# Kernel optimization log

Hardware: AMD Instinct MI355X
Metric: run time of the kernel (lower is better)

## Reference

```python
import jax, jax.numpy as jnp
import numpy as np

N_RAYS, MAX_S, N_VOX, EMB, HID, L_VIEW = 8192, 64, 100000, 32, 128, 4


def view_pe(d):
    # NeRF positional encoding of view dirs: [N,3] -> [N, 3 + 6*L_VIEW]
    freqs = 2.0 ** jnp.arange(L_VIEW, dtype=d.dtype)
    ang = (d[..., None] * freqs).reshape(*d.shape[:-1], -1)  # [N, 3*L]
    return jnp.concatenate([d, jnp.sin(ang), jnp.cos(ang)], -1)


def setup_inputs() -> dict:
    key = jax.random.key(0)
    ks = jax.random.split(key, 16)
    rays_d = jax.random.normal(ks[0], (N_RAYS, 3), dtype=jnp.float32)
    rays_d = rays_d / jnp.linalg.norm(rays_d, axis=-1, keepdims=True)
    pts = jax.random.uniform(ks[1], (N_RAYS, MAX_S, 3), dtype=jnp.float32)
    t_vals = jnp.sort(jax.random.uniform(ks[2], (N_RAYS, MAX_S), dtype=jnp.float32) * 4.0, axis=-1)
    dists = jnp.concatenate([t_vals[:, 1:] - t_vals[:, :-1], jnp.full((N_RAYS, 1), 0.05, jnp.float32)], -1)
    # ragged per-ray sample counts -> -1 padded p2v_idx (as produced by the voxel point sampler)
    counts = jax.random.randint(ks[3], (N_RAYS,), 1, MAX_S + 1)
    ray_hits = jax.random.bernoulli(ks[4], 0.9, (N_RAYS,))
    valid = (jnp.arange(MAX_S)[None, :] < counts[:, None]) & ray_hits[:, None]
    idx = jax.random.randint(ks[5], (N_RAYS, MAX_S), 0, N_VOX)
    p2v_idx = jnp.where(valid, idx, -1).astype(jnp.int32)

    def lin(k, i, o):
        return jax.random.normal(k, (i, o), dtype=jnp.float32) * np.float32(1.0 / np.sqrt(i))

    return dict(
        rays_d=rays_d, pts=pts, t_vals=t_vals, dists=dists,
        p2v_idx=p2v_idx, ray_hits=ray_hits,
        vox_emb=jax.random.normal(ks[6], (N_VOX, EMB), dtype=jnp.float32) * 0.1,
        Wpts=lin(ks[7], 3, EMB),
        W1=lin(ks[8], EMB, HID), b1=jnp.zeros((HID,), jnp.float32),
        W2=lin(ks[9], HID, HID), b2=jnp.zeros((HID,), jnp.float32),
        Wsig=lin(ks[10], HID, 1), bsig=jnp.zeros((1,), jnp.float32),
        Wfeat=lin(ks[11], HID, HID), bfeat=jnp.zeros((HID,), jnp.float32),
        Wc1=lin(ks[12], HID + 3 + 6 * L_VIEW, 64), bc1=jnp.zeros((64,), jnp.float32),
        Wc2=lin(ks[13], 64, 3), bc2=jnp.zeros((3,), jnp.float32),
    )


def reference(rays_d, pts, t_vals, dists, vox_emb, Wpts, W1, b1, W2, b2,
              Wsig, bsig, Wfeat, bfeat, Wc1, bc1, Wc2, bc2, p2v_idx, ray_hits):
    mask = p2v_idx >= 0                                   # [N,S] valid samples (mask_pts)
    idx = jnp.where(mask, p2v_idx, 0)
    # voxel_embedder: per-point voxel embedding gather + positional lift
    ve = vox_emb[idx] + pts @ Wpts                        # [N,S,EMB]
    h = jax.nn.relu(ve @ W1 + b1)
    h = jax.nn.relu(h @ W2 + b2)                          # [N,S,HID]
    sigma = (h @ Wsig + bsig)[..., 0]                     # [N,S]
    feat = h @ Wfeat + bfeat                              # [N,S,HID]
    vemb = view_pe(rays_d)                                # [N,27]
    vemb = jnp.broadcast_to(vemb[:, None, :], (feat.shape[0], feat.shape[1], vemb.shape[-1]))
    c = jax.nn.relu(jnp.concatenate([feat, vemb], -1) @ Wc1 + bc1)
    rgb_raw = c @ Wc2 + bc2                               # [N,S,3]
    # masked_scatter semantics: invalid slots are 0 before the min_color remap
    rgb = (jnp.where(mask[..., None], rgb_raw, 0.0) + 1.0) * 0.5   # min_color = -1
    free_energy = jnp.where(mask, jax.nn.relu(sigma) * dists, 0.0)  # [N,S]
    # volumetric_rendering(with_dist=True)
    shifted = jnp.concatenate([jnp.zeros_like(free_energy[:, :1]), free_energy[:, :-1]], -1)
    T = jnp.exp(-jnp.cumsum(shifted, -1))
    weights = (1.0 - jnp.exp(-free_energy)) * T           # [N,S]
    comp_rgb = jnp.einsum('ns,nsc->nc', weights, rgb)     # [N,3]
    acc = weights.sum(-1)                                 # [N]
    depth = (weights * t_vals).sum(-1)
    disp = 1.0 / jnp.maximum(1e-10, depth / jnp.maximum(acc, 1e-10))
    # fill_in for missed rays (white_bkgd=False -> fill with 0)
    comp_rgb = jnp.where(ray_hits[:, None], comp_rgb, 0.0)
    disp = jnp.where(ray_hits, disp, 0.0)
    acc = jnp.where(ray_hits, acc, 0.0)
    return comp_rgb, disp, acc
```

## Files before the change

### kernel.cpp

```cpp
#include <hip/hip_runtime.h>
#include <stdint.h>


#define NRAYS 8192
#define MAXS  64
#define EMB   32
#define HID   128
#define NPE   27
#define CH    64
#define NPTS  (NRAYS * MAXS)
#define RCAP  16384

#define WS_WCOMB  0
#define WS_WPE    (WS_WCOMB + HID*CH)
#define WS_BCOMB  (WS_WPE + 32*CH)
#define WS_CCINIT (WS_BCOMB + CH)
#define WS_COUNTS (WS_CCINIT + NRAYS*CH)
#define WS_OFFS   (WS_COUNTS + NRAYS)
#define WS_TOTAL  (WS_OFFS + NRAYS)
#define WS_RCNT   (WS_TOTAL + 1)
#define WS_LIST   (WS_TOTAL + 4)
#define WS_PTOUT  (WS_LIST + NPTS)
#define WS_FRAGS  (WS_PTOUT + 4*NPTS)
#define WS_RLIST  (WS_FRAGS + 56*2*64*4)
#define WS_PTSC   (WS_RLIST + RCAP)

typedef __attribute__((ext_vector_type(8))) short bf16x8;
typedef __attribute__((ext_vector_type(4))) float f32x4;
union FI { int i[4]; int4 v; bf16x8 f; };

#define MFMA16(a, b, c) __builtin_amdgcn_mfma_f32_16x16x32_bf16(a, b, c, 0, 0, 0)

__device__ __forceinline__ f32x4 mfma3(bf16x8 ah, bf16x8 al, bf16x8 bh, bf16x8 bl,
                                       f32x4 c) {
  c = MFMA16(al, bh, c);
  c = MFMA16(ah, bl, c);
  c = MFMA16(ah, bh, c);
  return c;
}

__device__ __forceinline__ f32x4 mfma2(bf16x8 ah, bf16x8 bh, bf16x8 bl, f32x4 c) {
  c = MFMA16(ah, bl, c);
  c = MFMA16(ah, bh, c);
  return c;
}

__device__ __forceinline__ void split8(const float* x, bf16x8& hi, bf16x8& lo) {
  FI H, L;
#pragma unroll
  for (int r = 0; r < 4; ++r) {
    unsigned u0 = __float_as_uint(x[2 * r]);
    unsigned u1 = __float_as_uint(x[2 * r + 1]);
    unsigned h0 = u0 & 0xffff0000u, h1 = u1 & 0xffff0000u;
    unsigned l0 = __float_as_uint(x[2 * r] - __uint_as_float(h0));
    unsigned l1 = __float_as_uint(x[2 * r + 1] - __uint_as_float(h1));
    H.i[r] = (int)((h0 >> 16) | (h1 & 0xffff0000u));
    L.i[r] = (int)((l0 >> 16) | (l1 & 0xffff0000u));
  }
  hi = H.f; lo = L.f;
}

__device__ __forceinline__ unsigned short bf16rne(float v) {
  unsigned u = __float_as_uint(v);
  return (unsigned short)((u + 0x7fffu + ((u >> 16) & 1u)) >> 16);
}

__global__ __launch_bounds__(256) void prep_kernel(
    const float* __restrict__ Wfeat, const float* __restrict__ bfeat,
    const float* __restrict__ Wc1, const float* __restrict__ bc1,
    float* __restrict__ ws) {
  int idx = blockIdx.x * 256 + threadIdx.x;
  if (idx < HID * CH) {
    int m = idx >> 6, j = idx & 63;
    float s = 0.f;
    for (int f = 0; f < HID; ++f) s = fmaf(Wfeat[m * HID + f], Wc1[f * CH + j], s);
    ws[WS_WCOMB + idx] = s;
    return;
  }
  idx -= HID * CH;
  if (idx < 32 * CH) {
    int v = idx >> 6, j = idx & 63;
    ws[WS_WPE + idx] = (v < NPE) ? Wc1[(HID + v) * CH + j] : 0.f;
    return;
  }
  idx -= 32 * CH;
  if (idx < CH) {
    float s = bc1[idx];
    for (int f = 0; f < HID; ++f) s = fmaf(bfeat[f], Wc1[f * CH + idx], s);
    ws[WS_BCOMB + idx] = s;
    return;
  }
  idx -= CH;
  if (idx < 2) ((int*)(ws + WS_TOTAL))[idx] = 0;
}

__global__ __launch_bounds__(256) void prep2_kernel(
    const float* __restrict__ W1, const float* __restrict__ W2,
    float* __restrict__ ws) {
  int t = blockIdx.x * 256 + threadIdx.x;
  if (t >= 56 * 64) return;
  const int fid = t >> 6, lane = t & 63;
  const int n16 = lane & 15, quad = lane >> 4;
  float x[8];
  if (fid < 8) {
    const int n = fid * 16 + n16, k0 = quad * 8;
#pragma unroll
    for (int j = 0; j < 8; ++j) x[j] = W1[(k0 + j) * HID + n];
  } else if (fid < 40) {
    const int f = fid - 8, nt = f >> 2, s = f & 3;
    const int n = nt * 16 + n16, k0 = s * 32 + quad * 8;
#pragma unroll
    for (int j = 0; j < 8; ++j) x[j] = W2[(k0 + j) * HID + n];
  } else {
    const int f = fid - 40, nt = f >> 2, s = f & 3;
    const int n = nt * 16 + n16, k0 = s * 32 + quad * 8;
#pragma unroll
    for (int j = 0; j < 8; ++j) x[j] = ws[WS_WCOMB + (k0 + j) * CH + n];
  }
  FI H, L;
#pragma unroll
  for (int r = 0; r < 4; ++r) {
    unsigned u0 = __float_as_uint(x[2 * r]);
    unsigned u1 = __float_as_uint(x[2 * r + 1]);
    unsigned h0 = u0 & 0xffff0000u, h1 = u1 & 0xffff0000u;
    unsigned l0 = __float_as_uint(x[2 * r] - __uint_as_float(h0));
    unsigned l1 = __float_as_uint(x[2 * r + 1] - __uint_as_float(h1));
    H.i[r] = (int)((h0 >> 16) | (h1 & 0xffff0000u));
    L.i[r] = (int)((l0 >> 16) | (l1 & 0xffff0000u));
  }
  int4* o = (int4*)(ws + WS_FRAGS);
  o[(fid * 2 + 0) * 64 + lane] = H.v;
  o[(fid * 2 + 1) * 64 + lane] = L.v;
}

__global__ __launch_bounds__(256) void count_pe_kernel(
    const float* __restrict__ rays_d, const int* __restrict__ p2v,
    float* __restrict__ ws) {
  const int tid = threadIdx.x;
  const int ray = blockIdx.x * 4 + (tid >> 6);
  const int lane = tid & 63;
  const int v = p2v[ray * MAXS + lane];
  const unsigned long long ball = __ballot(v >= 0);
  if (lane == 0) ((int*)(ws + WS_COUNTS))[ray] = __popcll(ball);

  const float d0 = rays_d[ray * 3 + 0];
  const float d1 = rays_d[ray * 3 + 1];
  const float d2 = rays_d[ray * 3 + 2];
  float vemb[NPE];
  vemb[0] = d0; vemb[1] = d1; vemb[2] = d2;
#pragma unroll
  for (int i = 0; i < 3; ++i) {
    const float di = (i == 0) ? d0 : (i == 1) ? d1 : d2;
#pragma unroll
    for (int l = 0; l < 4; ++l) {
      const float ang = di * (float)(1 << l);
      vemb[3 + i * 4 + l] = __sinf(ang);
      vemb[3 + 12 + i * 4 + l] = __cosf(ang);
    }
  }
  float s = ws[WS_BCOMB + lane];
  const float* wpe = ws + WS_WPE;
#pragma unroll
  for (int vv = 0; vv < NPE; ++vv) s = fmaf(vemb[vv], wpe[vv * CH + lane], s);
  ws[WS_CCINIT + ray * CH + lane] = s;
}

__global__ __launch_bounds__(1024) void scan_kernel(float* __restrict__ ws) {
  const int* counts = (const int*)(ws + WS_COUNTS);
  int* offs = (int*)(ws + WS_OFFS);
  int* totalp = (int*)(ws + WS_TOTAL);
  __shared__ int wsum[16];
  const int tid = threadIdx.x;
  const int lane = tid & 63;
  const int base = tid * 8;
  if (tid == 0) ((int*)(ws + WS_RCNT))[0] = 0;
  int c[8], e[8];
  int run = 0;
#pragma unroll
  for (int i = 0; i < 8; ++i) { c[i] = counts[base + i]; e[i] = run; run += c[i]; }
  int inc = run;
#pragma unroll
  for (int off = 1; off < 64; off <<= 1) {
    int u = __shfl_up(inc, off, 64);
    if (lane >= off) inc += u;
  }
  const int wexcl = inc - run;
  if (lane == 63) wsum[tid >> 6] = inc;
  __syncthreads();
  if (tid < 16) {
    int v = wsum[tid];
    int inc2 = v;
#pragma unroll
    for (int off = 1; off < 16; off <<= 1) {
      int u = __shfl_up(inc2, off, 64);
      if (tid >= off) inc2 += u;
    }
    wsum[tid] = inc2 - v;
    if (tid == 15) totalp[0] = inc2;
  }
  __syncthreads();
  const int wbase = wsum[tid >> 6];
#pragma unroll
  for (int i = 0; i < 8; ++i) offs[base + i] = wbase + wexcl + e[i];
}

__global__ __launch_bounds__(256) void list_kernel(
    const int* __restrict__ p2v, const float* __restrict__ pts,
    float* __restrict__ ws) {
  const int tid = threadIdx.x;
  const int ray = blockIdx.x * 4 + (tid >> 6);
  const int lane = tid & 63;
  const int pidx = ray * MAXS + lane;
  const int gidx = p2v[pidx];
  const bool valid = gidx >= 0;
  const unsigned long long ball = __ballot(valid);
  const int rank = __popcll(ball & ((1ull << lane) - 1ull));
  if (valid) {
    const int off = ((const int*)(ws + WS_OFFS))[ray];
    const int slot = off + rank;
    ((int*)(ws + WS_LIST))[slot] = pidx;
    float4 pc;
    pc.x = pts[pidx * 3 + 0];
    pc.y = pts[pidx * 3 + 1];
    pc.z = pts[pidx * 3 + 2];
    pc.w = __int_as_float(gidx);
    ((float4*)(ws + WS_PTSC))[slot] = pc;
  }
}

__device__ __forceinline__ void ve_frag(const float* __restrict__ vox_emb,
                                        const float* __restrict__ Wpts,
                                        float4 pc, int quad,
                                        bf16x8& hi, bf16x8& lo) {
  float x[8];
  const int gidx = __float_as_int(pc.w);
  const float4* vr = (const float4*)vox_emb + gidx * 8 + quad * 2;
  const float4 va = vr[0], vb = vr[1];
  const float px = pc.x, py = pc.y, pz = pc.z;
  const float4* wp = (const float4*)Wpts;
  const float4 wa0 = wp[quad * 2 + 0], wa1 = wp[quad * 2 + 1];
  const float4 wb0 = wp[8 + quad * 2 + 0], wb1 = wp[8 + quad * 2 + 1];
  const float4 wc0 = wp[16 + quad * 2 + 0], wc1 = wp[16 + quad * 2 + 1];
  x[0] = va.x + fmaf(px, wa0.x, fmaf(py, wb0.x, pz * wc0.x));
  x[1] = va.y + fmaf(px, wa0.y, fmaf(py, wb0.y, pz * wc0.y));
  x[2] = va.z + fmaf(px, wa0.z, fmaf(py, wb0.z, pz * wc0.z));
  x[3] = va.w + fmaf(px, wa0.w, fmaf(py, wb0.w, pz * wc0.w));
  x[4] = vb.x + fmaf(px, wa1.x, fmaf(py, wb1.x, pz * wc1.x));
  x[5] = vb.y + fmaf(px, wa1.y, fmaf(py, wb1.y, pz * wc1.y));
  x[6] = vb.z + fmaf(px, wa1.z, fmaf(py, wb1.z, pz * wc1.z));
  x[7] = vb.w + fmaf(px, wa1.w, fmaf(py, wb1.w, pz * wc1.w));
  split8(x, hi, lo);
}

#define SROW 136

__global__ __launch_bounds__(128, 2) void mlp_mfma(
    const float* __restrict__ vox_emb, const float* __restrict__ Wpts,
    const float* __restrict__ b1, const float* __restrict__ b2,
    const float* __restrict__ Wsig, const float* __restrict__ bsig,
    const float* __restrict__ Wc2, const float* __restrict__ bc2,
    float* __restrict__ ws) {
  __shared__ __align__(16) unsigned short alds[64 * SROW];
  const int tid = threadIdx.x;
  const int wave = tid >> 6, lane = tid & 63;
  const int n16 = lane & 15, quad = lane >> 4;
  const int total = ((const int*)(ws + WS_TOTAL))[0];
  const int base = blockIdx.x * 64 + wave * 32;
  if (base >= total) return;
  const int* list = (const int*)(ws + WS_LIST);
  const int slot0 = min(base + n16, total - 1);
  const int slot1 = min(base + 16 + n16, total - 1);
  const int pidx0 = list[slot0];
  const int pidx1 = list[slot1];
  const float4 pc0 = ((const float4*)(ws + WS_PTSC))[slot0];
  const float4 pc1 = ((const float4*)(ws + WS_PTSC))[slot1];
  const int4* fb = (const int4*)(ws + WS_FRAGS);

  int4 B1f[16];
#pragma unroll
  for (int i = 0; i < 16; ++i) B1f[i] = fb[i * 64 + lane];

  bf16x8 a0h, a0l, a1h, a1l;
  ve_frag(vox_emb, Wpts, pc0, quad, a0h, a0l);
  ve_frag(vox_emb, Wpts, pc1, quad, a1h, a1l);

  int4 BL[2][16];
#pragma unroll
  for (int nt = 0; nt < 8; ++nt) {
    BL[0][2 * nt]     = fb[((8 + nt * 4) * 2 + 0) * 64 + lane];
    BL[0][2 * nt + 1] = fb[((8 + nt * 4) * 2 + 1) * 64 + lane];
  }

  f32x4 h[2][8];
#pragma unroll
  for (int nt = 0; nt < 8; ++nt) {
    const float bb = b1[nt * 16 + n16];
    h[0][nt] = (f32x4){bb, bb, bb, bb};
    h[1][nt] = h[0][nt];
  }
#pragma unroll
  for (int nt = 0; nt < 8; ++nt) {
    FI H, L; H.v = B1f[2 * nt]; L.v = B1f[2 * nt + 1];
    h[0][nt] = mfma3(a0h, a0l, H.f, L.f, h[0][nt]);
    h[1][nt] = mfma3(a1h, a1l, H.f, L.f, h[1][nt]);
  }
#pragma unroll
  for (int mt = 0; mt < 2; ++mt)
#pragma unroll
    for (int nt = 0; nt < 8; ++nt)
#pragma unroll
      for (int r = 0; r < 4; ++r) {
        const float v = fmaxf(h[mt][nt][r], 0.f);
        const int row = wave * 32 + mt * 16 + quad * 4 + r;
        const int gk = ((2 * nt + (n16 >> 3)) ^ (row & 7)) << 3;
        alds[row * SROW + gk + (n16 & 7)] = bf16rne(v);
      }

  f32x4 g[2][8];
#pragma unroll
  for (int nt = 0; nt < 8; ++nt) {
    const float bb = b2[nt * 16 + n16];
    g[0][nt] = (f32x4){bb, bb, bb, bb};
    g[1][nt] = g[0][nt];
  }
  const int rrow0 = (wave * 32 + n16) * SROW;
  const int rrow1 = rrow0 + 16 * SROW;
  const int t7 = n16 & 7;
#pragma unroll
  for (int s = 0; s < 4; ++s) {
    if (s < 3) {
#pragma unroll
      for (int nt = 0; nt < 8; ++nt) {
        BL[(s + 1) & 1][2 * nt]     = fb[((8 + nt * 4 + s + 1) * 2 + 0) * 64 + lane];
        BL[(s + 1) & 1][2 * nt + 1] = fb[((8 + nt * 4 + s + 1) * 2 + 1) * 64 + lane];
      }
    }
    const int gq = ((4 * s + quad) ^ t7) << 3;
    const bf16x8 A0h = *(const bf16x8*)&alds[rrow0 + gq];
    const bf16x8 A1h = *(const bf16x8*)&alds[rrow1 + gq];
#pragma unroll
    for (int nt = 0; nt < 8; ++nt) {
      FI H, L; H.v = BL[s & 1][2 * nt]; L.v = BL[s & 1][2 * nt + 1];
      g[0][nt] = mfma2(A0h, H.f, L.f, g[0][nt]);
      g[1][nt] = mfma2(A1h, H.f, L.f, g[1][nt]);
    }
  }

  int pm[2][4];
#pragma unroll
  for (int mt = 0; mt < 2; ++mt)
#pragma unroll
    for (int r = 0; r < 4; ++r)
      pm[mt][r] = __shfl(mt ? pidx1 : pidx0, quad * 4 + r, 64);
  int4 BC[2][8];
#pragma unroll
  for (int nt = 0; nt < 4; ++nt) {
    BC[0][2 * nt]     = fb[((40 + nt * 4) * 2 + 0) * 64 + lane];
    BC[0][2 * nt + 1] = fb[((40 + nt * 4) * 2 + 1) * 64 + lane];
  }
  f32x4 cacc[2][4];
#pragma unroll
  for (int mt = 0; mt < 2; ++mt)
#pragma unroll
    for (int nt = 0; nt < 4; ++nt)
#pragma unroll
      for (int r = 0; r < 4; ++r)
        cacc[mt][nt][r] = ws[WS_CCINIT + (pm[mt][r] >> 6) * CH + nt * 16 + n16];

  float sg[2][4] = {{0.f, 0.f, 0.f, 0.f}, {0.f, 0.f, 0.f, 0.f}};
#pragma unroll
  for (int nt = 0; nt < 8; ++nt) {
    const float sv = Wsig[nt * 16 + n16];
#pragma unroll
    for (int mt = 0; mt < 2; ++mt)
#pragma unroll
      for (int r = 0; r < 4; ++r) {
        const float v = fmaxf(g[mt][nt][r], 0.f);
        sg[mt][r] = fmaf(v, sv, sg[mt][r]);
        const int row = wave * 32 + mt * 16 + quad * 4 + r;
        const int gk = ((2 * nt + (n16 >> 3)) ^ (row & 7)) << 3;
        alds[row * SROW + gk + (n16 & 7)] = bf16rne(v);
      }
  }
#pragma unroll
  for (int mask = 1; mask < 16; mask <<= 1)
#pragma unroll
    for (int mt = 0; mt < 2; ++mt)
#pragma unroll
      for (int r = 0; r < 4; ++r) sg[mt][r] += __shfl_xor(sg[mt][r], mask, 64);

#pragma unroll
  for (int s = 0; s < 4; ++s) {
    if (s < 3) {
#pragma unroll
      for (int nt = 0; nt < 4; ++nt) {
        BC[(s + 1) & 1][2 * nt]     = fb[((40 + nt * 4 + s + 1) * 2 + 0) * 64 + lane];
        BC[(s + 1) & 1][2 * nt + 1] = fb[((40 + nt * 4 + s + 1) * 2 + 1) * 64 + lane];
      }
    }
    const int gq = ((4 * s + quad) ^ t7) << 3;
    const bf16x8 A0h = *(const bf16x8*)&alds[rrow0 + gq];
    const bf16x8 A1h = *(const bf16x8*)&alds[rrow1 + gq];
#pragma unroll
    for (int nt = 0; nt < 4; ++nt) {
      FI H, L; H.v = BC[s & 1][2 * nt]; L.v = BC[s & 1][2 * nt + 1];
      cacc[0][nt] = mfma2(A0h, H.f, L.f, cacc[0][nt]);
      cacc[1][nt] = mfma2(A1h, H.f, L.f, cacc[1][nt]);
    }
  }

  float cr[2][3][4];
#pragma unroll
  for (int mt = 0; mt < 2; ++mt)
#pragma unroll
    for (int c = 0; c < 3; ++c)
#pragma unroll
      for (int r = 0; r < 4; ++r) cr[mt][c][r] = 0.f;
#pragma unroll
  for (int nt = 0; nt < 4; ++nt) {
    const int j = nt * 16 + n16;
    const float w0 = Wc2[j * 3 + 0], w1c = Wc2[j * 3 + 1], w2c = Wc2[j * 3 + 2];
#pragma unroll
    for (int mt = 0; mt < 2; ++mt)
#pragma unroll
      for (int r = 0; r < 4; ++r) {
        const float cv = fmaxf(cacc[mt][nt][r], 0.f);
        cr[mt][0][r] = fmaf(cv, w0, cr[mt][0][r]);
        cr[mt][1][r] = fmaf(cv, w1c, cr[mt][1][r]);
        cr[mt][2][r] = fmaf(cv, w2c, cr[mt][2][r]);
      }
  }
#pragma unroll
  for (int mask = 1; mask < 16; mask <<= 1)
#pragma unroll
    for (int mt = 0; mt < 2; ++mt)
#pragma unroll
      for (int c = 0; c < 3; ++c)
#pragma unroll
        for (int r = 0; r < 4; ++r) cr[mt][c][r] += __shfl_xor(cr[mt][c][r], mask, 64);

  if (n16 == 0) {
    const float bs = bsig[0];
    const float bcr = bc2[0], bcg = bc2[1], bcb = bc2[2];
#pragma unroll
    for (int mt = 0; mt < 2; ++mt)
#pragma unroll
      for (int r = 0; r < 4; ++r) {
        const int m = mt * 16 + quad * 4 + r;
        if (base + m < total) {
          const int pid = pm[mt][r];
          const float sig = sg[mt][r] + bs;
          ((float4*)(ws + WS_PTOUT))[pid] =
              make_float4(sig, cr[mt][0][r] + bcr, cr[mt][1][r] + bcg, cr[mt][2][r] + bcb);
          if (fabsf(sig) < 0.006f) {
            const int ri = atomicAdd((int*)(ws + WS_RCNT), 1);
            if (ri < RCAP) ((int*)(ws + WS_RLIST))[ri] = pid;
          }
        }
      }
  }
}

__device__ __forceinline__ float wave_sum(float v) {
#pragma unroll
  for (int off = 32; off > 0; off >>= 1) v += __shfl_down(v, off, 64);
  return v;
}

__global__ __launch_bounds__(256) void repair_kernel(
    const float* __restrict__ pts, const int* __restrict__ p2v,
    const float* __restrict__ vox_emb, const float* __restrict__ Wpts,
    const float* __restrict__ W1, const float* __restrict__ b1,
    const float* __restrict__ W2, const float* __restrict__ b2,
    const float* __restrict__ Wsig, const float* __restrict__ bsig,
    float* __restrict__ ws) {
  __shared__ float h1s[4][HID];
  const int wv = threadIdx.x >> 6, lane = threadIdx.x & 63;
  const int cnt = min(((const int*)(ws + WS_RCNT))[0], RCAP);
  const int nw = gridDim.x * 4;
  for (int i = blockIdx.x * 4 + wv; i < cnt; i += nw) {
    const int pidx = ((const int*)(ws + WS_RLIST))[i];
    const int gidx = p2v[pidx];
    const float px = pts[pidx * 3 + 0];
    const float py = pts[pidx * 3 + 1];
    const float pz = pts[pidx * 3 + 2];
    float ve[EMB];
#pragma unroll
    for (int e = 0; e < EMB; ++e)
      ve[e] = vox_emb[gidx * EMB + e] +
              fmaf(px, Wpts[e], fmaf(py, Wpts[EMB + e], pz * Wpts[2 * EMB + e]));
    float s0 = b1[lane], s1 = b1[lane + 64];
#pragma unroll
    for (int k = 0; k < EMB; ++k) {
      const float x = ve[k];
      s0 = fmaf(x, W1[k * HID + lane], s0);
      s1 = fmaf(x, W1[k * HID + lane + 64], s1);
    }
    h1s[wv][lane] = fmaxf(s0, 0.f);
    h1s[wv][lane + 64] = fmaxf(s1, 0.f);
    float t0 = b2[lane], t1 = b2[lane + 64];
    for (int k = 0; k < HID; ++k) {
      const float x = h1s[wv][k];
      t0 = fmaf(x, W2[k * HID + lane], t0);
      t1 = fmaf(x, W2[k * HID + lane + 64], t1);
    }
    float sp = fmaf(fmaxf(t0, 0.f), Wsig[lane], fmaxf(t1, 0.f) * Wsig[lane + 64]);
    sp = wave_sum(sp);
    if (lane == 0) ws[WS_PTOUT + 4 * pidx + 0] = sp + bsig[0];
  }
}

__device__ __forceinline__ float wave_prefix_excl(float v, int lane) {
  float inc = v;
#pragma unroll
  for (int off = 1; off < 64; off <<= 1) {
    float u = __shfl_up(inc, off, 64);
    if (lane >= off) inc += u;
  }
  return inc - v;
}

__global__ __launch_bounds__(256) void render_kernel(
    const float* __restrict__ t_vals, const float* __restrict__ dists,
    const int* __restrict__ p2v, const float* __restrict__ ws,
    float* __restrict__ out_rgb, float* __restrict__ out_disp,
    float* __restrict__ out_acc) {
  const int tid = threadIdx.x;
  const int ray = blockIdx.x * 4 + (tid >> 6);
  const int lane = tid & 63;
  const int pidx = ray * MAXS + lane;

  const int vidx = p2v[pidx];
  const bool hit = (__shfl(vidx, 0, 64) >= 0);
  if (!hit) {
    if (lane < 3) out_rgb[ray * 3 + lane] = 0.f;
    if (lane == 0) { out_disp[ray] = 0.f; out_acc[ray] = 0.f; }
    return;
  }
  const bool valid = vidx >= 0;

  const float4 pv = ((const float4*)(ws + WS_PTOUT))[pidx];
  const float fe = valid ? fmaxf(pv.x, 0.f) * dists[pidx] : 0.f;
  const float pref = wave_prefix_excl(fe, lane);
  const float T = __expf(-pref);
  const float w = (1.f - __expf(-fe)) * T;
  const float tv = t_vals[pidx];

  const float crgb0 = wave_sum(w * (pv.y + 1.f) * 0.5f);
  const float crgb1 = wave_sum(w * (pv.z + 1.f) * 0.5f);
  const float crgb2 = wave_sum(w * (pv.w + 1.f) * 0.5f);
  const float accs = wave_sum(w);
  const float depth = wave_sum(w * tv);

  if (lane == 0) {
    out_rgb[ray * 3 + 0] = crgb0;
    out_rgb[ray * 3 + 1] = crgb1;
    out_rgb[ray * 3 + 2] = crgb2;
    const float disp = 1.f / fmaxf(1e-10f, depth / fmaxf(accs, 1e-10f));
    out_disp[ray] = disp;
    out_acc[ray] = accs;
  }
}

extern "C" void kernel_launch(void* const* d_in, const int* in_sizes, int n_in,
                              void* d_out, int out_size, void* d_ws, size_t ws_size,
                              hipStream_t stream) {
  const float* rays_d  = (const float*)d_in[0];
  const float* pts     = (const float*)d_in[1];
  const float* t_vals  = (const float*)d_in[2];
  const float* dists   = (const float*)d_in[3];
  const int*   p2v     = (const int*)d_in[4];
  const float* vox_emb = (const float*)d_in[6];
  const float* Wpts    = (const float*)d_in[7];
  const float* W1      = (const float*)d_in[8];
  const float* b1      = (const float*)d_in[9];
  const float* W2      = (const float*)d_in[10];
  const float* b2      = (const float*)d_in[11];
  const float* Wsig    = (const float*)d_in[12];
  const float* bsig    = (const float*)d_in[13];
  const float* Wfeat   = (const float*)d_in[14];
  const float* bfeat   = (const float*)d_in[15];
  const float* Wc1     = (const float*)d_in[16];
  const float* bc1     = (const float*)d_in[17];
  const float* Wc2     = (const float*)d_in[18];
  const float* bc2     = (const float*)d_in[19];

  float* ws = (float*)d_ws;
  float* out = (float*)d_out;
  float* out_rgb = out;
  float* out_disp = out + NRAYS * 3;
  float* out_acc = out + NRAYS * 4;

  hipLaunchKernelGGL(prep_kernel, dim3(41), dim3(256), 0, stream,
                     Wfeat, bfeat, Wc1, bc1, ws);
  hipLaunchKernelGGL(prep2_kernel, dim3(14), dim3(256), 0, stream, W1, W2, ws);
  hipLaunchKernelGGL(count_pe_kernel, dim3(NRAYS / 4), dim3(256), 0, stream,
                     rays_d, p2v, ws);
  hipLaunchKernelGGL(scan_kernel, dim3(1), dim3(1024), 0, stream, ws);
  hipLaunchKernelGGL(list_kernel, dim3(NRAYS / 4), dim3(256), 0, stream,
                     p2v, pts, ws);
  hipLaunchKernelGGL(mlp_mfma, dim3(NPTS / 64), dim3(128), 0, stream,
                     vox_emb, Wpts, b1, b2, Wsig, bsig, Wc2, bc2, ws);
  hipLaunchKernelGGL(repair_kernel, dim3(128), dim3(256), 0, stream,
                     pts, p2v, vox_emb, Wpts, W1, b1, W2, b2, Wsig, bsig, ws);
  hipLaunchKernelGGL(render_kernel, dim3(NRAYS / 4), dim3(256), 0, stream,
                     t_vals, dists, p2v, ws, out_rgb, out_disp, out_acc);
}
```

Before: 255.5 us.

## Fuse preprocessing kernels and replace the scan with atomic per-ray compaction

Two weight-preparation kernels are merged into one: it now computes the Wfeat·Wc1 product directly while building the bf16 hi/lo MFMA fragments, skipping the fp32 intermediate round-trip. The per-ray count, single-block prefix scan and list-building kernels become one build kernel. Each wavefront reserves its ray's output slots with an atomicAdd on a global counter and also computes the view-encoding projection. This cuts the launch chain from five kernels to two and removes the serial scan. In exchange the compacted point order becomes non-deterministic across rays and per-ray offsets are no longer written.

Result: slower. 336.4 us (+31.7%).

```diff
diff --git a/kernel.cpp b/kernel.cpp
--- a/kernel.cpp
+++ b/kernel.cpp
@@ -66,18 +66,53 @@
 }
 
 __global__ __launch_bounds__(256) void prep_kernel(
+    const float* __restrict__ W1, const float* __restrict__ W2,
     const float* __restrict__ Wfeat, const float* __restrict__ bfeat,
     const float* __restrict__ Wc1, const float* __restrict__ bc1,
     float* __restrict__ ws) {
   int idx = blockIdx.x * 256 + threadIdx.x;
-  if (idx < HID * CH) {
-    int m = idx >> 6, j = idx & 63;
-    float s = 0.f;
-    for (int f = 0; f < HID; ++f) s = fmaf(Wfeat[m * HID + f], Wc1[f * CH + j], s);
-    ws[WS_WCOMB + idx] = s;
+  if (idx < 56 * 64) {
+    const int fid = idx >> 6, lane = idx & 63;
+    const int n16 = lane & 15, quad = lane >> 4;
+    float x[8];
+    if (fid < 8) {
+      const int n = fid * 16 + n16, k0 = quad * 8;
+#pragma unroll
+      for (int j = 0; j < 8; ++j) x[j] = W1[(k0 + j) * HID + n];
+    } else if (fid < 40) {
+      const int f = fid - 8, nt = f >> 2, s = f & 3;
+      const int n = nt * 16 + n16, k0 = s * 32 + quad * 8;
+#pragma unroll
+      for (int j = 0; j < 8; ++j) x[j] = W2[(k0 + j) * HID + n];
+    } else {
+      const int f = fid - 40, nt = f >> 2, s = f & 3;
+      const int n = nt * 16 + n16, k0 = s * 32 + quad * 8;
+#pragma unroll
+      for (int j = 0; j < 8; ++j) x[j] = 0.f;
+      for (int ff = 0; ff < HID; ++ff) {
+        const float wc = Wc1[ff * CH + n];
+#pragma unroll
+        for (int j = 0; j < 8; ++j)
+          x[j] = fmaf(Wfeat[(k0 + j) * HID + ff], wc, x[j]);
+      }
+    }
+    FI H, L;
+#pragma unroll
+    for (int r = 0; r < 4; ++r) {
+      unsigned u0 = __float_as_uint(x[2 * r]);
+      unsigned u1 = __float_as_uint(x[2 * r + 1]);
+      unsigned h0 = u0 & 0xffff0000u, h1 = u1 & 0xffff0000u;
+      unsigned l0 = __float_as_uint(x[2 * r] - __uint_as_float(h0));
+      unsigned l1 = __float_as_uint(x[2 * r + 1] - __uint_as_float(h1));
+      H.i[r] = (int)((h0 >> 16) | (h1 & 0xffff0000u));
+      L.i[r] = (int)((l0 >> 16) | (l1 & 0xffff0000u));
+    }
+    int4* o = (int4*)(ws + WS_FRAGS);
+    o[(fid * 2 + 0) * 64 + lane] = H.v;
+    o[(fid * 2 + 1) * 64 + lane] = L.v;
     return;
   }
-  idx -= HID * CH;
+  idx -= 56 * 64;
   if (idx < 32 * CH) {
     int v = idx >> 6, j = idx & 63;
     ws[WS_WPE + idx] = (v < NPE) ? Wc1[(HID + v) * CH + j] : 0.f;
@@ -94,119 +129,9 @@
   if (idx < 2) ((int*)(ws + WS_TOTAL))[idx] = 0;
 }
 
-__global__ __launch_bounds__(256) void prep2_kernel(
-    const float* __restrict__ W1, const float* __restrict__ W2,
-    float* __restrict__ ws) {
-  int t = blockIdx.x * 256 + threadIdx.x;
-  if (t >= 56 * 64) return;
-  const int fid = t >> 6, lane = t & 63;
-  const int n16 = lane & 15, quad = lane >> 4;
-  float x[8];
-  if (fid < 8) {
-    const int n = fid * 16 + n16, k0 = quad * 8;
-#pragma unroll
-    for (int j = 0; j < 8; ++j) x[j] = W1[(k0 + j) * HID + n];
-  } else if (fid < 40) {
-    const int f = fid - 8, nt = f >> 2, s = f & 3;
-    const int n = nt * 16 + n16, k0 = s * 32 + quad * 8;
-#pragma unroll
-    for (int j = 0; j < 8; ++j) x[j] = W2[(k0 + j) * HID + n];
-  } else {
-    const int f = fid - 40, nt = f >> 2, s = f & 3;
-    const int n = nt * 16 + n16, k0 = s * 32 + quad * 8;
-#pragma unroll
-    for (int j = 0; j < 8; ++j) x[j] = ws[WS_WCOMB + (k0 + j) * CH + n];
-  }
-  FI H, L;
-#pragma unroll
-  for (int r = 0; r < 4; ++r) {
-    unsigned u0 = __float_as_uint(x[2 * r]);
-    unsigned u1 = __float_as_uint(x[2 * r + 1]);
-    unsigned h0 = u0 & 0xffff0000u, h1 = u1 & 0xffff0000u;
-    unsigned l0 = __float_as_uint(x[2 * r] - __uint_as_float(h0));
-    unsigned l1 = __float_as_uint(x[2 * r + 1] - __uint_as_float(h1));
-    H.i[r] = (int)((h0 >> 16) | (h1 & 0xffff0000u));
-    L.i[r] = (int)((l0 >> 16) | (l1 & 0xffff0000u));
-  }
-  int4* o = (int4*)(ws + WS_FRAGS);
-  o[(fid * 2 + 0) * 64 + lane] = H.v;
-  o[(fid * 2 + 1) * 64 + lane] = L.v;
-}
-
-__global__ __launch_bounds__(256) void count_pe_kernel(
+__global__ __launch_bounds__(256) void build_kernel(
     const float* __restrict__ rays_d, const int* __restrict__ p2v,
-    float* __restrict__ ws) {
-  const int tid = threadIdx.x;
-  const int ray = blockIdx.x * 4 + (tid >> 6);
-  const int lane = tid & 63;
-  const int v = p2v[ray * MAXS + lane];
-  const unsigned long long ball = __ballot(v >= 0);
-  if (lane == 0) ((int*)(ws + WS_COUNTS))[ray] = __popcll(ball);
-
-  const float d0 = rays_d[ray * 3 + 0];
-  const float d1 = rays_d[ray * 3 + 1];
-  const float d2 = rays_d[ray * 3 + 2];
-  float vemb[NPE];
-  vemb[0] = d0; vemb[1] = d1; vemb[2] = d2;
-#pragma unroll
-  for (int i = 0; i < 3; ++i) {
-    const float di = (i == 0) ? d0 : (i == 1) ? d1 : d2;
-#pragma unroll
-    for (int l = 0; l < 4; ++l) {
-      const float ang = di * (float)(1 << l);
-      vemb[3 + i * 4 + l] = __sinf(ang);
-      vemb[3 + 12 + i * 4 + l] = __cosf(ang);
-    }
-  }
-  float s = ws[WS_BCOMB + lane];
-  const float* wpe = ws + WS_WPE;
-#pragma unroll
-  for (int vv = 0; vv < NPE; ++vv) s = fmaf(vemb[vv], wpe[vv * CH + lane], s);
-  ws[WS_CCINIT + ray * CH + lane] = s;
-}
-
-__global__ __launch_bounds__(1024) void scan_kernel(float* __restrict__ ws) {
-  const int* counts = (const int*)(ws + WS_COUNTS);
-  int* offs = (int*)(ws + WS_OFFS);
-  int* totalp = (int*)(ws + WS_TOTAL);
-  __shared__ int wsum[16];
-  const int tid = threadIdx.x;
-  const int lane = tid & 63;
-  const int base = tid * 8;
-  if (tid == 0) ((int*)(ws + WS_RCNT))[0] = 0;
-  int c[8], e[8];
-  int run = 0;
-#pragma unroll
-  for (int i = 0; i < 8; ++i) { c[i] = counts[base + i]; e[i] = run; run += c[i]; }
-  int inc = run;
-#pragma unroll
-  for (int off = 1; off < 64; off <<= 1) {
-    int u = __shfl_up(inc, off, 64);
-    if (lane >= off) inc += u;
-  }
-  const int wexcl = inc - run;
-  if (lane == 63) wsum[tid >> 6] = inc;
-  __syncthreads();
-  if (tid < 16) {
-    int v = wsum[tid];
-    int inc2 = v;
-#pragma unroll
-    for (int off = 1; off < 16; off <<= 1) {
-      int u = __shfl_up(inc2, off, 64);
-      if (tid >= off) inc2 += u;
-    }
-    wsum[tid] = inc2 - v;
-    if (tid == 15) totalp[0] = inc2;
-  }
-  __syncthreads();
-  const int wbase = wsum[tid >> 6];
-#pragma unroll
-  for (int i = 0; i < 8; ++i) offs[base + i] = wbase + wexcl + e[i];
-}
-
-__global__ __launch_bounds__(256) void list_kernel(
-    const int* __restrict__ p2v, const float* __restrict__ pts,
-    float* __restrict__ ws) {
+    const float* __restrict__ pts, float* __restrict__ ws) {
   const int tid = threadIdx.x;
   const int ray = blockIdx.x * 4 + (tid >> 6);
   const int lane = tid & 63;
@@ -214,9 +139,13 @@
   const int gidx = p2v[pidx];
   const bool valid = gidx >= 0;
   const unsigned long long ball = __ballot(valid);
+  const int cnt = __popcll(ball);
   const int rank = __popcll(ball & ((1ull << lane) - 1ull));
+  int off = 0;
+  if (lane == 0 && cnt > 0)
+    off = atomicAdd((int*)(ws + WS_TOTAL), cnt);
+  off = __shfl(off, 0, 64);
   if (valid) {
-    const int off = ((const int*)(ws + WS_OFFS))[ray];
     const int slot = off + rank;
     ((int*)(ws + WS_LIST))[slot] = pidx;
     float4 pc;
@@ -226,6 +155,27 @@
     pc.w = __int_as_float(gidx);
     ((float4*)(ws + WS_PTSC))[slot] = pc;
   }
+
+  const float d0 = rays_d[ray * 3 + 0];
+  const float d1 = rays_d[ray * 3 + 1];
+  const float d2 = rays_d[ray * 3 + 2];
+  float vemb[NPE];
+  vemb[0] = d0; vemb[1] = d1; vemb[2] = d2;
+#pragma unroll
+  for (int i = 0; i < 3; ++i) {
+    const float di = (i == 0) ? d0 : (i == 1) ? d1 : d2;
+#pragma unroll
+    for (int l = 0; l < 4; ++l) {
+      const float ang = di * (float)(1 << l);
+      vemb[3 + i * 4 + l] = __sinf(ang);
+      vemb[3 + 12 + i * 4 + l] = __cosf(ang);
+    }
+  }
+  float s = ws[WS_BCOMB + lane];
+  const float* wpe = ws + WS_WPE;
+#pragma unroll
+  for (int vv = 0; vv < NPE; ++vv) s = fmaf(vemb[vv], wpe[vv * CH + lane], s);
+  ws[WS_CCINIT + ray * CH + lane] = s;
 }
 
 __device__ __forceinline__ void ve_frag(const float* __restrict__ vox_emb,
@@ -591,14 +541,10 @@
   float* out_disp = out + NRAYS * 3;
   float* out_acc = out + NRAYS * 4;
 
-  hipLaunchKernelGGL(prep_kernel, dim3(41), dim3(256), 0, stream,
-                     Wfeat, bfeat, Wc1, bc1, ws);
-  hipLaunchKernelGGL(prep2_kernel, dim3(14), dim3(256), 0, stream, W1, W2, ws);
-  hipLaunchKernelGGL(count_pe_kernel, dim3(NRAYS / 4), dim3(256), 0, stream,
-                     rays_d, p2v, ws);
-  hipLaunchKernelGGL(scan_kernel, dim3(1), dim3(1024), 0, stream, ws);
-  hipLaunchKernelGGL(list_kernel, dim3(NRAYS / 4), dim3(256), 0, stream,
-                     p2v, pts, ws);
+  hipLaunchKernelGGL(prep_kernel, dim3(23), dim3(256), 0, stream,
+                     W1, W2, Wfeat, bfeat, Wc1, bc1, ws);
+  hipLaunchKernelGGL(build_kernel, dim3(NRAYS / 4), dim3(256), 0, stream,
+                     rays_d, p2v, pts, ws);
   hipLaunchKernelGGL(mlp_mfma, dim3(NPTS / 64), dim3(128), 0, stream,
                      vox_emb, Wpts, b1, b2, Wsig, bsig, Wc2, bc2, ws);
   hipLaunchKernelGGL(repair_kernel, dim3(128), dim3(256), 0, stream,
```
